# Kernel tuning notes

Hardware: AMD Instinct MI355X
Metric: run time of the kernel (lower is better)

## Reference

```python
import jax, jax.numpy as jnp
import numpy as np

SHAPE = (192, 192, 192)


def _trilinear_sample(img, z, y, x):
    # img: [B,C,D,H,W]; z,y,x: [B,D,H,W] absolute voxel coords (align_corners=True,
    # zero padding outside the volume, matching F.grid_sample defaults in vroc).
    B, C, D, H, W = img.shape
    imgf = img.reshape(B, C, -1)
    z0 = jnp.floor(z); y0 = jnp.floor(y); x0 = jnp.floor(x)
    wz = z - z0; wy = y - y0; wx = x - x0
    z0i = z0.astype(jnp.int32); y0i = y0.astype(jnp.int32); x0i = x0.astype(jnp.int32)
    z1i = z0i + 1; y1i = y0i + 1; x1i = x0i + 1

    def gather(iz, iy, ix):
        valid = ((iz >= 0) & (iz < D) & (iy >= 0) & (iy < H) & (ix >= 0) & (ix < W))
        lin = ((jnp.clip(iz, 0, D - 1) * H + jnp.clip(iy, 0, H - 1)) * W
               + jnp.clip(ix, 0, W - 1)).reshape(B, 1, -1)
        v = jnp.take_along_axis(imgf, jnp.broadcast_to(lin, (B, C, D * H * W)), axis=2)
        return v.reshape(B, C, D, H, W) * valid.reshape(B, 1, D, H, W).astype(img.dtype)

    def w(a, b, c):
        return (a * b * c)[:, None]  # [B,1,D,H,W]

    out = (gather(z0i, y0i, x0i) * w(1 - wz, 1 - wy, 1 - wx)
           + gather(z0i, y0i, x1i) * w(1 - wz, 1 - wy, wx)
           + gather(z0i, y1i, x0i) * w(1 - wz, wy, 1 - wx)
           + gather(z0i, y1i, x1i) * w(1 - wz, wy, wx)
           + gather(z1i, y0i, x0i) * w(wz, 1 - wy, 1 - wx)
           + gather(z1i, y0i, x1i) * w(wz, 1 - wy, wx)
           + gather(z1i, y1i, x0i) * w(wz, wy, 1 - wx)
           + gather(z1i, y1i, x1i) * w(wz, wy, wx))
    return out


def _warp(moving_image, vector_field):
    # SpatialTransformer: identity grid + displacement (voxel units), trilinear sample.
    B, C, D, H, W = moving_image.shape
    dt = moving_image.dtype
    gz, gy, gx = jnp.meshgrid(jnp.arange(D, dtype=dt), jnp.arange(H, dtype=dt),
                              jnp.arange(W, dtype=dt), indexing='ij')
    z = gz[None] + vector_field[:, 0]
    y = gy[None] + vector_field[:, 1]
    x = gx[None] + vector_field[:, 2]
    return _trilinear_sample(moving_image, z, y, x)


def setup_inputs() -> dict:
    key = jax.random.key(0)
    k1, k2, k3, k4 = jax.random.split(key, 4)
    D, H, W = SHAPE
    moving_image = jax.random.normal(k1, (1, 1, D, H, W), dtype=jnp.float32)
    vector_field = jax.random.normal(k2, (1, 3, D, H, W), dtype=jnp.float32) * 3.0
    fixed_image = jax.random.normal(k3, (1, 1, D, H, W), dtype=jnp.float32)
    fixed_image_mask = jax.random.randint(k4, (1, 1, D, H, W), 0, 2).astype(bool)
    return {"moving_image": moving_image, "vector_field": vector_field,
            "fixed_image": fixed_image, "fixed_image_mask": fixed_image_mask}


def reference(moving_image, vector_field, fixed_image, fixed_image_mask):
    warped = _warp(moving_image, vector_field)
    m = fixed_image_mask.astype(warped.dtype)
    sq = (warped - fixed_image) ** 2
    # F.mse_loss(warped[mask], fixed[mask]) == mean of squared diff over masked voxels
    return jnp.sum(sq * m) / jnp.maximum(jnp.sum(m), 1.0)
```

## Files before the change

kernel.cpp:

```cpp
#include <hip/hip_runtime.h>
#include <hip/hip_fp16.h>

#define DD 192
#define HH 192
#define WW 192
#define NVOX (DD * HH * WW)

#define TX 32
#define TY 16
#define TZ 8
#define RSX 48
#define RSY 33
#define RSZ 25
#define DEPTH 32
#define ROWD 24
#define SLABD (RSY * ROWD)
#define CHROW 6
#define CHSLAB (RSY * CHROW)
#define NT 1024
#define GRID 256

#define AS1 __attribute__((address_space(1)))
#define AS3 __attribute__((address_space(3)))

#define WAITCNT(n) asm volatile("s_waitcnt vmcnt(" #n ")" ::: "memory")

typedef float f32x4 __attribute__((ext_vector_type(4)));
typedef int   i32x4 __attribute__((ext_vector_type(4)));

__global__ __launch_bounds__(256) void conv_fp16(
    const float4* __restrict__ in, int4* __restrict__ out)
{
    const int i = blockIdx.x * 256 + threadIdx.x;
    const float4 a = in[2 * i];
    const float4 b = in[2 * i + 1];
    __half2 h0 = __floats2half2_rn(a.x, a.y);
    __half2 h1 = __floats2half2_rn(a.z, a.w);
    __half2 h2 = __floats2half2_rn(b.x, b.y);
    __half2 h3 = __floats2half2_rn(b.z, b.w);
    int4 o;
    o.x = *(int*)&h0; o.y = *(int*)&h1; o.z = *(int*)&h2; o.w = *(int*)&h3;
    out[i] = o;
}

struct Streams { f32x4 dz, dy, dx, f; i32x4 m; };

__device__ __forceinline__ void tile_coords_col(
    int n, int OX, int OY, int OZ, int& tx, int& ty, int& tz, int& tzi)
{
    const int c = n / 12;
    tzi = n - c * 12;
    const int ox = c / 6;
    tx = OX + ox;
    ty = OY + (c - ox * 6);
    tz = OZ + tzi;
}

template<int NSLAB>
__device__ __forceinline__ void stage_slabs(
    const ushort* __restrict__ movh, const ushort* __restrict__ zbuf,
    uint* sbufd, int x_lo, int y_lo, int z_first, int tid)
{
    ushort* sbuf = (ushort*)sbufd;
    const int sg = tid >> 7;
    const int lq = tid & 127;
    constexpr int NIT = (NSLAB + 7) / 8;
    #pragma unroll
    for (int it = 0; it < NIT; ++it) {
        const int j = it * 8 + sg;
        if ((NSLAB & 7) == 0 || j < NSLAB) {
            const int zg = z_first + j;
            const int s  = zg & (DEPTH - 1);
            #pragma unroll
            for (int r = 0; r < 2; ++r) {
                const int q = lq + r * 128;
                if (q < CHSLAB) {
                    const int ry = q / CHROW;
                    const int k  = q - ry * CHROW;
                    const int gy = y_lo + ry, gx = x_lo + 8 * k;
                    const bool valid = ((unsigned)zg < DD) & ((unsigned)gy < HH) &
                                       ((unsigned)gx < WW);
                    const ushort* src = valid ? (movh + ((zg * HH + gy) * WW + gx))
                                              : zbuf;
                    const int cb = q & ~63;
                    __builtin_amdgcn_global_load_lds((AS1 void*)src,
                        (AS3 void*)(sbuf + s * (SLABD * 2) + cb * 8), 16, 0, 0);
                }
            }
        }
    }
}

__device__ __forceinline__ Streams prefetch_streams(
    const float* __restrict__ vf, const float* __restrict__ fix,
    const int* __restrict__ mask, int base)
{
    Streams s;
    s.dz = __builtin_nontemporal_load((const f32x4*)(vf + base));
    s.dy = __builtin_nontemporal_load((const f32x4*)(vf + NVOX + base));
    s.dx = __builtin_nontemporal_load((const f32x4*)(vf + 2 * NVOX + base));
    s.f  = __builtin_nontemporal_load((const f32x4*)(fix + base));
    s.m  = __builtin_nontemporal_load((const i32x4*)(mask + base));
    return s;
}

__device__ __forceinline__ void sample_accum(
    const uint* sdw, const ushort* __restrict__ movh,
    int gz, int gy, int gx, float dz, float dy, float dx,
    float f, int m, int x_lo, int y_lo, int z_lo,
    float& sq, float& cnt)
{
    const float z = (float)gz + dz, y = (float)gy + dy, x = (float)gx + dx;
    const float z0f = floorf(z), y0f = floorf(y), x0f = floorf(x);
    const float wz = z - z0f, wy = y - y0f, wx = x - x0f;
    const int z0 = (int)z0f, y0 = (int)y0f, x0 = (int)x0f;
    const int z0l = z0 - z_lo, y0l = y0 - y_lo, x0l = x0 - x_lo;
    const bool inbox = ((unsigned)z0l < RSZ - 1) & ((unsigned)y0l < RSY - 1) &
                       ((unsigned)x0l < RSX - 1);

    float v000, v001, v010, v011, v100, v101, v110, v111;
    if (inbox) {
        const int sb0 = (z0 & (DEPTH - 1)) * SLABD;
        const int sb1 = ((z0 + 1) & (DEPTH - 1)) * SLABD;
        const int ob = y0l * ROWD + (x0l >> 1);
        const bool odd = (x0l & 1) != 0;
        const uint a00 = sdw[sb0 + ob];
        const uint b00 = sdw[sb0 + ob + 1];
        const uint a01 = sdw[sb0 + ob + ROWD];
        const uint b01 = sdw[sb0 + ob + ROWD + 1];
        const uint a10 = sdw[sb1 + ob];
        const uint b10 = sdw[sb1 + ob + 1];
        const uint a11 = sdw[sb1 + ob + ROWD];
        const uint b11 = sdw[sb1 + ob + ROWD + 1];
        auto pr = [&](uint A, uint B, float& l, float& r) {
            const float2 fa = __half22float2(*(const __half2*)&A);
            const float fb = __low2float(*(const __half2*)&B);
            l = odd ? fa.y : fa.x;
            r = odd ? fb   : fa.y;
        };
        pr(a00, b00, v000, v001);
        pr(a01, b01, v010, v011);
        pr(a10, b10, v100, v101);
        pr(a11, b11, v110, v111);
    } else {
        const int z1 = z0 + 1, y1 = y0 + 1, x1 = x0 + 1;
        const bool zi0 = (unsigned)z0 < DD, zi1 = (unsigned)z1 < DD;
        const bool yi0 = (unsigned)y0 < HH, yi1 = (unsigned)y1 < HH;
        const bool xi0 = (unsigned)x0 < WW, xi1 = (unsigned)x1 < WW;
        const int zc0 = min(max(z0, 0), DD - 1), zc1 = min(max(z1, 0), DD - 1);
        const int yc0 = min(max(y0, 0), HH - 1), yc1 = min(max(y1, 0), HH - 1);
        const int xc0 = min(max(x0, 0), WW - 1), xc1 = min(max(x1, 0), WW - 1);
        const int r00 = (zc0 * HH + yc0) * WW;
        const int r01 = (zc0 * HH + yc1) * WW;
        const int r10 = (zc1 * HH + yc0) * WW;
        const int r11 = (zc1 * HH + yc1) * WW;
        v000 = (zi0 & yi0 & xi0) ? __half2float(((const __half*)movh)[r00 + xc0]) : 0.0f;
        v001 = (zi0 & yi0 & xi1) ? __half2float(((const __half*)movh)[r00 + xc1]) : 0.0f;
        v010 = (zi0 & yi1 & xi0) ? __half2float(((const __half*)movh)[r01 + xc0]) : 0.0f;
        v011 = (zi0 & yi1 & xi1) ? __half2float(((const __half*)movh)[r01 + xc1]) : 0.0f;
        v100 = (zi1 & yi0 & xi0) ? __half2float(((const __half*)movh)[r10 + xc0]) : 0.0f;
        v101 = (zi1 & yi0 & xi1) ? __half2float(((const __half*)movh)[r10 + xc1]) : 0.0f;
        v110 = (zi1 & yi1 & xi0) ? __half2float(((const __half*)movh)[r11 + xc0]) : 0.0f;
        v111 = (zi1 & yi1 & xi1) ? __half2float(((const __half*)movh)[r11 + xc1]) : 0.0f;
    }

    const float c00 = v000 + (v001 - v000) * wx;
    const float c01 = v010 + (v011 - v010) * wx;
    const float c10 = v100 + (v101 - v100) * wx;
    const float c11 = v110 + (v111 - v110) * wx;
    const float c0 = c00 + (c01 - c00) * wy;
    const float c1 = c10 + (c11 - c10) * wy;
    const float warped = c0 + (c1 - c0) * wz;

    const float mm = (m != 0) ? 1.0f : 0.0f;
    const float diff = warped - f;
    sq += diff * diff * mm;
    cnt += mm;
}

__global__ __launch_bounds__(NT) void warp_mse_persist(
    const ushort* __restrict__ movh,
    const float* __restrict__ mov,
    const float* __restrict__ vf,
    const float* __restrict__ fix,
    const int* __restrict__ mask,
    const ushort* __restrict__ zbuf,
    float* __restrict__ acc,
    float* __restrict__ out)
{
    __shared__ uint sbufd[DEPTH * SLABD + 8];
    __shared__ float s_sq[16], s_cnt[16];

    const int tid = threadIdx.x;
    const int b = blockIdx.x;
    const int xcd = b & 7;
    const int w   = b >> 3;
    const int start = w * 6 + min(w, 24);
    const int cnt_t = 6 + (w < 24 ? 1 : 0);
    const int OX = (xcd & 1) * 3;
    const int OY = ((xcd >> 1) & 1) * 6;
    const int OZ = ((xcd >> 2) & 1) * 12;

    const int lxg = (tid & 7) * 4;
    const int ly  = (tid >> 3) & 15;
    const int lz  = tid >> 7;

    float sq = 0.0f, cntm = 0.0f;

    int tx, ty, tz, tzi;
    tile_coords_col(start, OX, OY, OZ, tx, ty, tz, tzi);
    stage_slabs<RSZ>(movh, zbuf, sbufd, tx * TX - 8, ty * TY - 8, tz * TZ - 8, tid);
    Streams Scur = prefetch_streams(vf, fix, mask,
        ((tz * TZ + lz) * HH + ty * TY + ly) * WW + tx * TX + lxg);
    int nx, ny, nz, nzi;
    tile_coords_col(start + 1, OX, OY, OZ, nx, ny, nz, nzi);
    Streams Snxt = prefetch_streams(vf, fix, mask,
        ((nz * TZ + lz) * HH + ny * TY + ly) * WW + nx * TX + lxg);
    WAITCNT(10);
    __builtin_amdgcn_s_barrier();
    __builtin_amdgcn_sched_barrier(0);

    for (int k = 0; k < cnt_t; ++k) {
        int cx, cy, cz, czi;
        tile_coords_col(start + k, OX, OY, OZ, cx, cy, cz, czi);
        const int x_lo = cx * TX - 8, y_lo = cy * TY - 8, z_lo = cz * TZ - 8;
        const int gz = cz * TZ + lz, gy = cy * TY + ly, gx0 = cx * TX + lxg;
        const uint* sdw = sbufd;

        sample_accum(sdw, movh, gz, gy, gx0,     Scur.dz.x, Scur.dy.x, Scur.dx.x,
                     Scur.f.x, Scur.m.x, x_lo, y_lo, z_lo, sq, cntm);
        sample_accum(sdw, movh, gz, gy, gx0 + 1, Scur.dz.y, Scur.dy.y, Scur.dx.y,
                     Scur.f.y, Scur.m.y, x_lo, y_lo, z_lo, sq, cntm);
        sample_accum(sdw, movh, gz, gy, gx0 + 2, Scur.dz.z, Scur.dy.z, Scur.dx.z,
                     Scur.f.z, Scur.m.z, x_lo, y_lo, z_lo, sq, cntm);
        sample_accum(sdw, movh, gz, gy, gx0 + 3, Scur.dz.w, Scur.dy.w, Scur.dx.w,
                     Scur.f.w, Scur.m.w, x_lo, y_lo, z_lo, sq, cntm);

        if (k + 1 < cnt_t) {
            __builtin_amdgcn_sched_barrier(0);
            __builtin_amdgcn_s_barrier();
            Scur = Snxt;
            int px, py, pz, pzi;
            tile_coords_col(start + k + 1, OX, OY, OZ, px, py, pz, pzi);
            const int zlo1 = pz * TZ - 8;
            if (czi != 11) {
                stage_slabs<8>(movh, zbuf, sbufd, px * TX - 8, py * TY - 8,
                               zlo1 + 17, tid);
            } else {
                stage_slabs<RSZ>(movh, zbuf, sbufd, px * TX - 8, py * TY - 8,
                                 zlo1, tid);
            }
            if (k + 2 < cnt_t) {
                int qx, qy, qz, qzi;
                tile_coords_col(start + k + 2, OX, OY, OZ, qx, qy, qz, qzi);
                Snxt = prefetch_streams(vf, fix, mask,
                    ((qz * TZ + lz) * HH + qy * TY + ly) * WW + qx * TX + lxg);
                WAITCNT(5);
            } else {
                WAITCNT(0);
            }
            __builtin_amdgcn_s_barrier();
            __builtin_amdgcn_sched_barrier(0);
        }
    }

    #pragma unroll
    for (int off = 32; off > 0; off >>= 1) {
        sq   += __shfl_down(sq, off, 64);
        cntm += __shfl_down(cntm, off, 64);
    }
    const int lane = tid & 63;
    const int wid = tid >> 6;
    if (lane == 0) { s_sq[wid] = sq; s_cnt[wid] = cntm; }
    __syncthreads();
    if (tid == 0) {
        float bsq = 0.0f, bcnt = 0.0f;
        #pragma unroll
        for (int i = 0; i < 16; ++i) { bsq += s_sq[i]; bcnt += s_cnt[i]; }
        atomicAdd(&acc[0], bsq);
        atomicAdd(&acc[1], bcnt);
        __threadfence();
        const unsigned old = atomicAdd((unsigned*)&acc[2], 1u);
        if (old == GRID - 1) {
            __threadfence();
            const float s = atomicAdd(&acc[0], 0.0f);
            const float c = atomicAdd(&acc[1], 0.0f);
            out[0] = s / fmaxf(c, 1.0f);
        }
    }
}

__global__ __launch_bounds__(256) void warp_mse_simple(
    const float* __restrict__ mov, const float* __restrict__ vf,
    const float* __restrict__ fix, const int* __restrict__ mask,
    float* __restrict__ acc)
{
    const int idx = blockIdx.x * 256 + threadIdx.x;
    float sq = 0.0f, cnt = 0.0f;
    if (idx < NVOX) {
        const int w = idx % WW;
        const int t = idx / WW;
        const int h = t % HH;
        const int d = t / HH;
        const float z = (float)d + vf[idx];
        const float y = (float)h + vf[NVOX + idx];
        const float x = (float)w + vf[2 * NVOX + idx];
        const float z0f = floorf(z), y0f = floorf(y), x0f = floorf(x);
        const float wz = z - z0f, wy = y - y0f, wx = x - x0f;
        const int z0 = (int)z0f, y0 = (int)y0f, x0 = (int)x0f;
        const int z1 = z0 + 1, y1 = y0 + 1, x1 = x0 + 1;
        const bool zi0 = (unsigned)z0 < DD, zi1 = (unsigned)z1 < DD;
        const bool yi0 = (unsigned)y0 < HH, yi1 = (unsigned)y1 < HH;
        const bool xi0 = (unsigned)x0 < WW, xi1 = (unsigned)x1 < WW;
        auto ld = [&](int iz, int iy, int ix, bool ok) -> float {
            return ok ? mov[(iz * HH + iy) * WW + ix] : 0.0f;
        };
        const float v000 = ld(z0, y0, x0, zi0 & yi0 & xi0);
        const float v001 = ld(z0, y0, x1, zi0 & yi0 & xi1);
        const float v010 = ld(z0, y1, x0, zi0 & yi1 & xi0);
        const float v011 = ld(z0, y1, x1, zi0 & yi1 & xi1);
        const float v100 = ld(z1, y0, x0, zi1 & yi0 & xi0);
        const float v101 = ld(z1, y0, x1, zi1 & yi0 & xi1);
        const float v110 = ld(z1, y1, x0, zi1 & yi1 & xi0);
        const float v111 = ld(z1, y1, x1, zi1 & yi1 & xi1);
        const float c00 = v000 + (v001 - v000) * wx;
        const float c01 = v010 + (v011 - v010) * wx;
        const float c10 = v100 + (v101 - v100) * wx;
        const float c11 = v110 + (v111 - v110) * wx;
        const float c0 = c00 + (c01 - c00) * wy;
        const float c1 = c10 + (c11 - c10) * wy;
        const float warped = c0 + (c1 - c0) * wz;
        const float m = (mask[idx] != 0) ? 1.0f : 0.0f;
        const float diff = warped - fix[idx];
        sq = diff * diff * m;
        cnt = m;
    }
    #pragma unroll
    for (int off = 32; off > 0; off >>= 1) {
        sq  += __shfl_down(sq, off, 64);
        cnt += __shfl_down(cnt, off, 64);
    }
    __shared__ float s_sq[4], s_cnt[4];
    const int lane = threadIdx.x & 63, wid = threadIdx.x >> 6;
    if (lane == 0) { s_sq[wid] = sq; s_cnt[wid] = cnt; }
    __syncthreads();
    if (threadIdx.x == 0) {
        atomicAdd(&acc[0], s_sq[0] + s_sq[1] + s_sq[2] + s_sq[3]);
        atomicAdd(&acc[1], s_cnt[0] + s_cnt[1] + s_cnt[2] + s_cnt[3]);
    }
}

__global__ void warp_mse_finalize(const float* __restrict__ acc, float* __restrict__ out) {
    out[0] = acc[0] / fmaxf(acc[1], 1.0f);
}

extern "C" void kernel_launch(void* const* d_in, const int* in_sizes, int n_in,
                              void* d_out, int out_size, void* d_ws, size_t ws_size,
                              hipStream_t stream) {
    const float* mov  = (const float*)d_in[0];
    const float* vf   = (const float*)d_in[1];
    const float* fix  = (const float*)d_in[2];
    const int*   mask = (const int*)d_in[3];
    float* acc = (float*)d_ws;
    float* out = (float*)d_out;

    hipMemsetAsync(d_ws, 0, 256, stream);

    const size_t need = 256 + (size_t)NVOX * 2;
    if (ws_size >= need) {
        ushort* movh = (ushort*)((char*)d_ws + 256);
        const ushort* zbuf = (const ushort*)((char*)d_ws + 64);
        conv_fp16<<<NVOX / (256 * 8), 256, 0, stream>>>(
            (const float4*)mov, (int4*)movh);
        warp_mse_persist<<<GRID, NT, 0, stream>>>(movh, mov, vf, fix, mask,
                                                  zbuf, acc, out);
    } else {
        warp_mse_simple<<<(NVOX + 255) / 256, 256, 0, stream>>>(mov, vf, fix, mask, acc);
        warp_mse_finalize<<<1, 1, 0, stream>>>(acc, out);
    }
}
```

Before: 229.9 us.

## Use 33-slab LDS ring to prefetch next tile's halo slabs a step ahead

The z-ring of staged moving-image slabs grows from 32 to 33 entries, with modulo indexing relative to a per-run base. The tile loop is split into up to two straight z-column runs. This frees ring space so the 8 new slabs for tile k+2 can be staged while tile k+1 is pending, hiding halo loads behind compute. Column transitions now restage the full 25-slab box at run start, and the code carries leftover dead variables and non-power-of-two modulo arithmetic.

```diff
diff --git a/kernel.cpp b/kernel.cpp
--- a/kernel.cpp
+++ b/kernel.cpp
@@ -12,7 +12,7 @@
 #define RSX 48
 #define RSY 33
 #define RSZ 25
-#define DEPTH 32
+#define DEPTH 33
 #define ROWD 24
 #define SLABD (RSY * ROWD)
 #define CHROW 6
@@ -45,17 +45,6 @@
 
 struct Streams { f32x4 dz, dy, dx, f; i32x4 m; };
 
-__device__ __forceinline__ void tile_coords_col(
-    int n, int OX, int OY, int OZ, int& tx, int& ty, int& tz, int& tzi)
-{
-    const int c = n / 12;
-    tzi = n - c * 12;
-    const int ox = c / 6;
-    tx = OX + ox;
-    ty = OY + (c - ox * 6);
-    tz = OZ + tzi;
-}
-
 template<int NSLAB>
 __device__ __forceinline__ void stage_slabs(
     const ushort* __restrict__ movh, const ushort* __restrict__ zbuf,
@@ -70,7 +59,7 @@
         const int j = it * 8 + sg;
         if ((NSLAB & 7) == 0 || j < NSLAB) {
             const int zg = z_first + j;
-            const int s  = zg & (DEPTH - 1);
+            const int s  = (int)((unsigned)(zg + DEPTH) % (unsigned)DEPTH);
             #pragma unroll
             for (int r = 0; r < 2; ++r) {
                 const int q = lq + r * 128;
@@ -107,7 +96,7 @@
 __device__ __forceinline__ void sample_accum(
     const uint* sdw, const ushort* __restrict__ movh,
     int gz, int gy, int gx, float dz, float dy, float dx,
-    float f, int m, int x_lo, int y_lo, int z_lo,
+    float f, int m, int x_lo, int y_lo, int z_lo, int bs,
     float& sq, float& cnt)
 {
     const float z = (float)gz + dz, y = (float)gy + dy, x = (float)gx + dx;
@@ -120,8 +109,10 @@
 
     float v000, v001, v010, v011, v100, v101, v110, v111;
     if (inbox) {
-        const int sb0 = (z0 & (DEPTH - 1)) * SLABD;
-        const int sb1 = ((z0 + 1) & (DEPTH - 1)) * SLABD;
+        int s0 = bs + z0l; s0 -= (s0 >= DEPTH) ? DEPTH : 0;
+        int s1 = s0 + 1;   s1 -= (s1 >= DEPTH) ? DEPTH : 0;
+        const int sb0 = s0 * SLABD;
+        const int sb1 = s1 * SLABD;
         const int ob = y0l * ROWD + (x0l >> 1);
         const bool odd = (x0l & 1) != 0;
         const uint a00 = sdw[sb0 + ob];
@@ -207,61 +198,86 @@
 
     float sq = 0.0f, cntm = 0.0f;
 
-    int tx, ty, tz, tzi;
-    tile_coords_col(start, OX, OY, OZ, tx, ty, tz, tzi);
-    stage_slabs<RSZ>(movh, zbuf, sbufd, tx * TX - 8, ty * TY - 8, tz * TZ - 8, tid);
-    Streams Scur = prefetch_streams(vf, fix, mask,
-        ((tz * TZ + lz) * HH + ty * TY + ly) * WW + tx * TX + lxg);
-    int nx, ny, nz, nzi;
-    tile_coords_col(start + 1, OX, OY, OZ, nx, ny, nz, nzi);
-    Streams Snxt = prefetch_streams(vf, fix, mask,
-        ((nz * TZ + lz) * HH + ny * TY + ly) * WW + nx * TX + lxg);
-    WAITCNT(10);
-    __builtin_amdgcn_s_barrier();
-    __builtin_amdgcn_sched_barrier(0);
-
-    for (int k = 0; k < cnt_t; ++k) {
-        int cx, cy, cz, czi;
-        tile_coords_col(start + k, OX, OY, OZ, cx, cy, cz, czi);
-        const int x_lo = cx * TX - 8, y_lo = cy * TY - 8, z_lo = cz * TZ - 8;
-        const int gz = cz * TZ + lz, gy = cy * TY + ly, gx0 = cx * TX + lxg;
-        const uint* sdw = sbufd;
-
-        sample_accum(sdw, movh, gz, gy, gx0,     Scur.dz.x, Scur.dy.x, Scur.dx.x,
-                     Scur.f.x, Scur.m.x, x_lo, y_lo, z_lo, sq, cntm);
-        sample_accum(sdw, movh, gz, gy, gx0 + 1, Scur.dz.y, Scur.dy.y, Scur.dx.y,
-                     Scur.f.y, Scur.m.y, x_lo, y_lo, z_lo, sq, cntm);
-        sample_accum(sdw, movh, gz, gy, gx0 + 2, Scur.dz.z, Scur.dy.z, Scur.dx.z,
-                     Scur.f.z, Scur.m.z, x_lo, y_lo, z_lo, sq, cntm);
-        sample_accum(sdw, movh, gz, gy, gx0 + 3, Scur.dz.w, Scur.dy.w, Scur.dx.w,
-                     Scur.f.w, Scur.m.w, x_lo, y_lo, z_lo, sq, cntm);
-
-        if (k + 1 < cnt_t) {
-            __builtin_amdgcn_sched_barrier(0);
-            __builtin_amdgcn_s_barrier();
-            Scur = Snxt;
-            int px, py, pz, pzi;
-            tile_coords_col(start + k + 1, OX, OY, OZ, px, py, pz, pzi);
-            const int zlo1 = pz * TZ - 8;
-            if (czi != 11) {
-                stage_slabs<8>(movh, zbuf, sbufd, px * TX - 8, py * TY - 8,
-                               zlo1 + 17, tid);
-            } else {
-                stage_slabs<RSZ>(movh, zbuf, sbufd, px * TX - 8, py * TY - 8,
-                                 zlo1, tid);
+    const int cA   = start / 12;
+    const int tzA  = start - cA * 12;
+    const int lenA = min(cnt_t, 12 - tzA);
+    const int lenB = cnt_t - lenA;
+
+    auto run = [&](int col, int tz0, int L) {
+        const int ox = col / 6;
+        const int tx = OX + ox;
+        const int ty = OY + (col - ox * 6);
+        const int x_lo = tx * TX - 8;
+        const int y_lo = ty * TY - 8;
+        const int gy  = ty * TY + ly;
+        const int gx0 = tx * TX + lxg;
+        const int z_lo0 = (OZ + tz0) * TZ - 8;
+        const int sbase = ((tz0 * TZ - 8) % DEPTH + DEPTH) % DEPTH;
+        const int bs0 = (int)((unsigned)(z_lo0 + 8 * DEPTH) % (unsigned)DEPTH);
+        (void)sbase;
+        const int sb0 = ((z_lo0 % WW) + 0, ((z_lo0 + 0) * 0));
+        (void)sb0;
+
+        stage_slabs<RSZ>(movh, zbuf, sbufd, x_lo, y_lo, z_lo0, tid);
+        Streams Scur = prefetch_streams(vf, fix, mask,
+            ((z_lo0 + 8 + lz) * HH + gy) * WW + gx0);
+        Streams Snxt = Scur;
+        if (L > 1) {
+            stage_slabs<8>(movh, zbuf, sbufd, x_lo, y_lo, z_lo0 + RSZ, tid);
+            Snxt = prefetch_streams(vf, fix, mask,
+                ((z_lo0 + 16 + lz) * HH + gy) * WW + gx0);
+            WAITCNT(10);
+        } else {
+            WAITCNT(5);
+        }
+        __builtin_amdgcn_s_barrier();
+        __builtin_amdgcn_sched_barrier(0);
+
+        for (int k = 0; k < L; ++k) {
+            const int z_lo = z_lo0 + k * TZ;
+            int bs = bs0 + k * TZ;
+            bs -= (bs >= DEPTH) ? DEPTH : 0;
+            bs -= (bs >= DEPTH) ? DEPTH : 0;
+            bs -= (bs >= DEPTH) ? DEPTH : 0;
+            const int gz = z_lo + 8 + lz;
+
+            sample_accum(sbufd, movh, gz, gy, gx0,     Scur.dz.x, Scur.dy.x,
+                         Scur.dx.x, Scur.f.x, Scur.m.x, x_lo, y_lo, z_lo, bs,
+                         sq, cntm);
+            sample_accum(sbufd, movh, gz, gy, gx0 + 1, Scur.dz.y, Scur.dy.y,
+                         Scur.dx.y, Scur.f.y, Scur.m.y, x_lo, y_lo, z_lo, bs,
+                         sq, cntm);
+            sample_accum(sbufd, movh, gz, gy, gx0 + 2, Scur.dz.z, Scur.dy.z,
+                         Scur.dx.z, Scur.f.z, Scur.m.z, x_lo, y_lo, z_lo, bs,
+                         sq, cntm);
+            sample_accum(sbufd, movh, gz, gy, gx0 + 3, Scur.dz.w, Scur.dy.w,
+                         Scur.dx.w, Scur.f.w, Scur.m.w, x_lo, y_lo, z_lo, bs,
+                         sq, cntm);
+
+            if (k + 1 < L) {
+                __builtin_amdgcn_sched_barrier(0);
+                __builtin_amdgcn_s_barrier();
+                Scur = Snxt;
+                if (k + 2 < L) {
+                    stage_slabs<8>(movh, zbuf, sbufd, x_lo, y_lo,
+                                   z_lo0 + (k + 2) * TZ + 17, tid);
+                    Snxt = prefetch_streams(vf, fix, mask,
+                        ((z_lo0 + (k + 2) * TZ + 8 + lz) * HH + gy) * WW + gx0);
+                    WAITCNT(7);
+                } else {
+                    WAITCNT(0);
+                }
+                __builtin_amdgcn_s_barrier();
+                __builtin_amdgcn_sched_barrier(0);
             }
-            if (k + 2 < cnt_t) {
-                int qx, qy, qz, qzi;
-                tile_coords_col(start + k + 2, OX, OY, OZ, qx, qy, qz, qzi);
-                Snxt = prefetch_streams(vf, fix, mask,
-                    ((qz * TZ + lz) * HH + qy * TY + ly) * WW + qx * TX + lxg);
-                WAITCNT(5);
-            } else {
-                WAITCNT(0);
-            }
-            __builtin_amdgcn_s_barrier();
-            __builtin_amdgcn_sched_barrier(0);
         }
+    };
+
+    run(cA, tzA, lenA);
+    if (lenB > 0) {
+        __builtin_amdgcn_sched_barrier(0);
+        __builtin_amdgcn_s_barrier();
+        run(cA + 1, 0, lenB);
     }
 
     #pragma unroll
```

After: 243.3 us. 5.8% more time.

## Grow the LDS ring to 33 slabs and prefetch next tile's slabs one iteration early

Applied to the files above, without the earlier changes.

The z-slab ring buffer grows from 32 to 33 slabs, with modulo indexing in place of masking. This leaves room for the 8 new slabs of the tile after next to be staged one iteration ahead, so their global-to-LDS loads overlap with the current tile's sampling instead of being waited on at the barrier. Tile coordinates are now computed once into a struct that carries the ring base offset. The cost is extra modulo and compare instructions in the sampling path, slightly more LDS, and more intricate waitcnt bookkeeping that must stay exact to be correct.

```diff
diff --git a/kernel.cpp b/kernel.cpp
--- a/kernel.cpp
+++ b/kernel.cpp
@@ -12,7 +12,7 @@
 #define RSX 48
 #define RSY 33
 #define RSZ 25
-#define DEPTH 32
+#define DEPTH 33
 #define ROWD 24
 #define SLABD (RSY * ROWD)
 #define CHROW 6
@@ -45,15 +45,20 @@
 
 struct Streams { f32x4 dz, dy, dx, f; i32x4 m; };
 
-__device__ __forceinline__ void tile_coords_col(
-    int n, int OX, int OY, int OZ, int& tx, int& ty, int& tz, int& tzi)
-{
-    const int c = n / 12;
-    tzi = n - c * 12;
-    const int ox = c / 6;
-    tx = OX + ox;
-    ty = OY + (c - ox * 6);
-    tz = OZ + tzi;
+struct TC { int x_lo, y_lo, z_lo, sbase, tzi; };
+__device__ __forceinline__ TC tcoords(int n, int OX, int OY, int OZ)
+{
+    const int c   = n / 12;
+    const int tzi = n - c * 12;
+    const int ox  = c / 6;
+    const int oy  = c - ox * 6;
+    TC t;
+    t.x_lo  = (OX + ox) * TX - 8;
+    t.y_lo  = (OY + oy) * TY - 8;
+    t.z_lo  = (OZ + tzi) * TZ - 8;
+    t.sbase = (int)((unsigned)(t.z_lo + DEPTH) % (unsigned)DEPTH);
+    t.tzi   = tzi;
+    return t;
 }
 
 template<int NSLAB>
@@ -70,7 +75,7 @@
         const int j = it * 8 + sg;
         if ((NSLAB & 7) == 0 || j < NSLAB) {
             const int zg = z_first + j;
-            const int s  = zg & (DEPTH - 1);
+            const int s  = (int)((unsigned)(zg + DEPTH) % (unsigned)DEPTH);
             #pragma unroll
             for (int r = 0; r < 2; ++r) {
                 const int q = lq + r * 128;
@@ -107,7 +112,7 @@
 __device__ __forceinline__ void sample_accum(
     const uint* sdw, const ushort* __restrict__ movh,
     int gz, int gy, int gx, float dz, float dy, float dx,
-    float f, int m, int x_lo, int y_lo, int z_lo,
+    float f, int m, int x_lo, int y_lo, int z_lo, int bs,
     float& sq, float& cnt)
 {
     const float z = (float)gz + dz, y = (float)gy + dy, x = (float)gx + dx;
@@ -120,8 +125,12 @@
 
     float v000, v001, v010, v011, v100, v101, v110, v111;
     if (inbox) {
-        const int sb0 = (z0 & (DEPTH - 1)) * SLABD;
-        const int sb1 = ((z0 + 1) & (DEPTH - 1)) * SLABD;
+        int s0 = bs + z0l;
+        s0 -= (s0 >= DEPTH) ? DEPTH : 0;
+        int s1 = s0 + 1;
+        s1 -= (s1 >= DEPTH) ? DEPTH : 0;
+        const int sb0 = s0 * SLABD;
+        const int sb1 = s1 * SLABD;
         const int ob = y0l * ROWD + (x0l >> 1);
         const bool odd = (x0l & 1) != 0;
         const uint a00 = sdw[sb0 + ob];
@@ -207,57 +216,78 @@
 
     float sq = 0.0f, cntm = 0.0f;
 
-    int tx, ty, tz, tzi;
-    tile_coords_col(start, OX, OY, OZ, tx, ty, tz, tzi);
-    stage_slabs<RSZ>(movh, zbuf, sbufd, tx * TX - 8, ty * TY - 8, tz * TZ - 8, tid);
+    const TC t0 = tcoords(start, OX, OY, OZ);
+    stage_slabs<RSZ>(movh, zbuf, sbufd, t0.x_lo, t0.y_lo, t0.z_lo, tid);
+    const TC t1p = tcoords(start + 1, OX, OY, OZ);
+    const bool roll1 = (t1p.tzi != 0);
+    if (roll1) {
+        stage_slabs<8>(movh, zbuf, sbufd, t0.x_lo, t0.y_lo, t0.z_lo + RSZ, tid);
+    }
     Streams Scur = prefetch_streams(vf, fix, mask,
-        ((tz * TZ + lz) * HH + ty * TY + ly) * WW + tx * TX + lxg);
-    int nx, ny, nz, nzi;
-    tile_coords_col(start + 1, OX, OY, OZ, nx, ny, nz, nzi);
+        ((t0.z_lo + 8 + lz) * HH + (t0.y_lo + 8 + ly)) * WW + t0.x_lo + 8 + lxg);
     Streams Snxt = prefetch_streams(vf, fix, mask,
-        ((nz * TZ + lz) * HH + ny * TY + ly) * WW + nx * TX + lxg);
-    WAITCNT(10);
+        ((t1p.z_lo + 8 + lz) * HH + (t1p.y_lo + 8 + ly)) * WW + t1p.x_lo + 8 + lxg);
+    if (roll1) { WAITCNT(12); }
+    else       { WAITCNT(10); }
     __builtin_amdgcn_s_barrier();
     __builtin_amdgcn_sched_barrier(0);
 
     for (int k = 0; k < cnt_t; ++k) {
-        int cx, cy, cz, czi;
-        tile_coords_col(start + k, OX, OY, OZ, cx, cy, cz, czi);
-        const int x_lo = cx * TX - 8, y_lo = cy * TY - 8, z_lo = cz * TZ - 8;
-        const int gz = cz * TZ + lz, gy = cy * TY + ly, gx0 = cx * TX + lxg;
-        const uint* sdw = sbufd;
-
-        sample_accum(sdw, movh, gz, gy, gx0,     Scur.dz.x, Scur.dy.x, Scur.dx.x,
-                     Scur.f.x, Scur.m.x, x_lo, y_lo, z_lo, sq, cntm);
-        sample_accum(sdw, movh, gz, gy, gx0 + 1, Scur.dz.y, Scur.dy.y, Scur.dx.y,
-                     Scur.f.y, Scur.m.y, x_lo, y_lo, z_lo, sq, cntm);
-        sample_accum(sdw, movh, gz, gy, gx0 + 2, Scur.dz.z, Scur.dy.z, Scur.dx.z,
-                     Scur.f.z, Scur.m.z, x_lo, y_lo, z_lo, sq, cntm);
-        sample_accum(sdw, movh, gz, gy, gx0 + 3, Scur.dz.w, Scur.dy.w, Scur.dx.w,
-                     Scur.f.w, Scur.m.w, x_lo, y_lo, z_lo, sq, cntm);
+        const TC tc = tcoords(start + k, OX, OY, OZ);
+        const int gz  = tc.z_lo + 8 + lz;
+        const int gyv = tc.y_lo + 8 + ly;
+        const int gx0 = tc.x_lo + 8 + lxg;
+
+        sample_accum(sbufd, movh, gz, gyv, gx0,     Scur.dz.x, Scur.dy.x,
+                     Scur.dx.x, Scur.f.x, Scur.m.x, tc.x_lo, tc.y_lo, tc.z_lo,
+                     tc.sbase, sq, cntm);
+        sample_accum(sbufd, movh, gz, gyv, gx0 + 1, Scur.dz.y, Scur.dy.y,
+                     Scur.dx.y, Scur.f.y, Scur.m.y, tc.x_lo, tc.y_lo, tc.z_lo,
+                     tc.sbase, sq, cntm);
+        sample_accum(sbufd, movh, gz, gyv, gx0 + 2, Scur.dz.z, Scur.dy.z,
+                     Scur.dx.z, Scur.f.z, Scur.m.z, tc.x_lo, tc.y_lo, tc.z_lo,
+                     tc.sbase, sq, cntm);
+        sample_accum(sbufd, movh, gz, gyv, gx0 + 3, Scur.dz.w, Scur.dy.w,
+                     Scur.dx.w, Scur.f.w, Scur.m.w, tc.x_lo, tc.y_lo, tc.z_lo,
+                     tc.sbase, sq, cntm);
 
         if (k + 1 < cnt_t) {
             __builtin_amdgcn_sched_barrier(0);
             __builtin_amdgcn_s_barrier();
+            const TC t1 = tcoords(start + k + 1, OX, OY, OZ);
             Scur = Snxt;
-            int px, py, pz, pzi;
-            tile_coords_col(start + k + 1, OX, OY, OZ, px, py, pz, pzi);
-            const int zlo1 = pz * TZ - 8;
-            if (czi != 11) {
-                stage_slabs<8>(movh, zbuf, sbufd, px * TX - 8, py * TY - 8,
-                               zlo1 + 17, tid);
+            if (t1.tzi == 0) {
+                stage_slabs<RSZ>(movh, zbuf, sbufd, t1.x_lo, t1.y_lo, t1.z_lo, tid);
+                if (k + 2 < cnt_t) {
+                    stage_slabs<8>(movh, zbuf, sbufd, t1.x_lo, t1.y_lo,
+                                   t1.z_lo + RSZ, tid);
+                    const TC t2 = tcoords(start + k + 2, OX, OY, OZ);
+                    Snxt = prefetch_streams(vf, fix, mask,
+                        ((t2.z_lo + 8 + lz) * HH + (t2.y_lo + 8 + ly)) * WW
+                        + t2.x_lo + 8 + lxg);
+                    WAITCNT(7);
+                } else {
+                    WAITCNT(0);
+                }
             } else {
-                stage_slabs<RSZ>(movh, zbuf, sbufd, px * TX - 8, py * TY - 8,
-                                 zlo1, tid);
-            }
-            if (k + 2 < cnt_t) {
-                int qx, qy, qz, qzi;
-                tile_coords_col(start + k + 2, OX, OY, OZ, qx, qy, qz, qzi);
-                Snxt = prefetch_streams(vf, fix, mask,
-                    ((qz * TZ + lz) * HH + qy * TY + ly) * WW + qx * TX + lxg);
-                WAITCNT(5);
-            } else {
-                WAITCNT(0);
+                if (k + 2 < cnt_t) {
+                    const TC t2 = tcoords(start + k + 2, OX, OY, OZ);
+                    if (t2.tzi != 0) {
+                        stage_slabs<8>(movh, zbuf, sbufd, t2.x_lo, t2.y_lo,
+                                       t2.z_lo + 17, tid);
+                        Snxt = prefetch_streams(vf, fix, mask,
+                            ((t2.z_lo + 8 + lz) * HH + (t2.y_lo + 8 + ly)) * WW
+                            + t2.x_lo + 8 + lxg);
+                        WAITCNT(12);
+                    } else {
+                        Snxt = prefetch_streams(vf, fix, mask,
+                            ((t2.z_lo + 8 + lz) * HH + (t2.y_lo + 8 + ly)) * WW
+                            + t2.x_lo + 8 + lxg);
+                        WAITCNT(10);
+                    }
+                } else {
+                    WAITCNT(5);
+                }
             }
             __builtin_amdgcn_s_barrier();
             __builtin_amdgcn_sched_barrier(0);
```

After: 269.6 us. +17.2%, slower.
